# Kernel optimization log

Hardware: AMD Instinct MI355X
Metric: run time of the kernel (lower is better)

## Reference

```python
import jax, jax.numpy as jnp
import numpy as np

N = 4096   # atoms
B = 64     # structures in batch
K = 128    # k-vectors per structure
E = 256    # emb_size_atom
D = 8      # downprojection_size
NUM_HIDDEN = 3


def _silu(x):
    return x * jax.nn.sigmoid(x)


def _residual(x, W):
    # ResidualLayer: two bias-free Dense(E,E) with SiLU, plus skip
    y = _silu(x @ W[0].T)
    y = _silu(y @ W[1].T)
    return x + y


def setup_inputs() -> dict:
    key = jax.random.key(0)
    ks = jax.random.split(key, 10)
    h = jax.random.normal(ks[0], (N, E), jnp.float32)
    x = jax.random.uniform(ks[1], (N, 3), jnp.float32) * 10.0  # Angstrom-scale positions
    k = jax.random.normal(ks[2], (B, K, 3), jnp.float32)
    batch_seg = jnp.sort(jax.random.randint(ks[3], (N,), 0, B))
    sc = 1.0 / np.sqrt(E)
    W_pre = jax.random.normal(ks[4], (2, E, E), jnp.float32) * sc        # pre_residual
    W_down = jax.random.normal(ks[5], (D, K), jnp.float32) / np.sqrt(K)  # shared downprojection (D,K)
    W_up = jax.random.normal(ks[6], (E, D), jnp.float32) / np.sqrt(D)    # up (E,D)
    W0 = jax.random.normal(ks[7], (E, E), jnp.float32) * sc              # first dense of ewald_layers
    W_res = jax.random.normal(ks[8], (NUM_HIDDEN, 2, E, E), jnp.float32) * sc
    return {"h": h, "x": x, "k": k, "batch_seg": batch_seg, "num_batch": B,
            "W_pre": W_pre, "W_down": W_down, "W_up": W_up, "W0": W0, "W_res": W_res}


def reference(h, x, k, batch_seg, num_batch, W_pre, W_down, W_up, W0, W_res):
    hres = _residual(h, W_pre)                       # (N,E)
    # dot products of atom positions with their structure's k-vectors
    dot = jnp.einsum('nkd,nd->nk', k[batch_seg], x)  # (N,K); sinc_damping == 1 (use_pbc)
    c, s = jnp.cos(dot), jnp.sin(dot)
    # structure factors: scatter-sum over atoms within each structure
    sf_real = jax.ops.segment_sum(hres[:, None, :] * c[:, :, None], batch_seg,
                                  num_segments=num_batch)  # (B,K,E)
    sf_imag = jax.ops.segment_sum(hres[:, None, :] * s[:, :, None], batch_seg,
                                  num_segments=num_batch)  # (B,K,E)
    # low-rank learned Fourier-space filter (use_pbc branch)
    kfilter = (W_up @ W_down).T                      # (K,E)
    # re-project filtered structure factors back to atoms
    h_update = 0.01 * jnp.sum(
        (sf_real * kfilter)[batch_seg] * c[:, :, None]
        + (sf_imag * kfilter)[batch_seg] * s[:, :, None], axis=1)  # (N,E)
    # ewald_layers update MLP: Dense + num_hidden residual blocks
    hu = _silu(h_update @ W0.T)
    for i in range(NUM_HIDDEN):
        hu = _residual(hu, W_res[i])
    return hu, dot
```

## Files before the change

kernel.cpp:

```cpp
#include <hip/hip_runtime.h>

#define NN 4096
#define BB 64
#define KK 128
#define EE 256
#define HTS 4352
#define CSR 4224
#define PCAP 160
#define YTS 264
#define ZTS 20

typedef unsigned short u16;
typedef __bf16 bhalf;
typedef bhalf bhalf8 __attribute__((ext_vector_type(8)));
typedef float floatx4 __attribute__((ext_vector_type(4)));

__device__ __forceinline__ float b2f(u16 u) {
  union { unsigned int i; float f; } v; v.i = ((unsigned int)u) << 16; return v.f;
}
__device__ __forceinline__ u16 f2b(float f) {
  union { float f; unsigned int i; } v; v.f = f;
  unsigned int r = (v.i + 0x7FFFu + ((v.i >> 16) & 1u)) >> 16;
  return (u16)r;
}
__device__ __forceinline__ float silu_f(float v) {
  return v / (1.f + __expf(-v));
}
__device__ __forceinline__ bhalf8 ld8f(const float* __restrict__ p) {
  float4 f0 = *(const float4*)p;
  float4 f1 = *(const float4*)(p + 4);
  union { bhalf8 v; u16 s[8]; } u;
  u.s[0] = f2b(f0.x); u.s[1] = f2b(f0.y); u.s[2] = f2b(f0.z); u.s[3] = f2b(f0.w);
  u.s[4] = f2b(f1.x); u.s[5] = f2b(f1.y); u.s[6] = f2b(f1.z); u.s[7] = f2b(f1.w);
  return u.v;
}


__global__ __launch_bounds__(256) void p1_k(
    const float* __restrict__ Wpre, const float* __restrict__ W0,
    const float* __restrict__ Wres, const float* __restrict__ Wup,
    const float* __restrict__ Wdn, const int* __restrict__ bs,
    const float* __restrict__ x, const float* __restrict__ kvec,
    u16* __restrict__ wpre, u16* __restrict__ w0b, u16* __restrict__ wrb,
    float* __restrict__ kft, u16* __restrict__ csb,
    int* __restrict__ seg, float* __restrict__ dout)
{
  int bid = blockIdx.x, tid = threadIdx.x;
  if (bid < 288) {
    int mat = bid >> 5;
    int w8 = ((bid & 31) * 256 + tid);
    int o = w8 * 8;
    int lane = w8 & 63, k = (w8 >> 6) & 7, nt = w8 >> 9;
    int r = lane & 15, q = lane >> 4;
    int src = (nt * 16 + r) * 256 + q * 8 + k * 32;
    const float* S; u16* D;
    if (mat < 2)      { S = Wpre + mat * 65536;       D = wpre + mat * 65536; }
    else if (mat == 2){ S = W0;                       D = w0b; }
    else              { S = Wres + (mat - 3) * 65536; D = wrb + (mat - 3) * 65536; }
    *(bhalf8*)(D + o) = ld8f(S + src);
  }
  else if (bid < 416) {
    int i = (bid - 288) * 256 + tid;
    int e = i >> 7, kk = i & 127;
    float a = 0.f;
#pragma unroll
    for (int d = 0; d < 8; ++d) a += Wup[e * 8 + d] * Wdn[d * KK + kk];
    kft[i] = a;
  } else if (bid < 424) {
    int base = 4096 * 256 + ((bid - 416) * 256 + tid) * 16;
    uint4 z = {0, 0, 0, 0};
    *(uint4*)(csb + base) = z;
    *(uint4*)(csb + base + 8) = z;
  } else if (bid == 424) {
    int b = tid;
    if (b <= BB) {
      int lo = 0, hi = NN;
      while (lo < hi) { int mid = (lo + hi) >> 1; if (bs[mid] < b) lo = mid + 1; else hi = mid; }
      seg[b] = lo;
    }
  } else {
    int i = (bid - 425) * 256 + tid;
    int n = i >> 7, kk = i & 127;
    int b = bs[n];
    const float* kp = kvec + (b * KK + kk) * 3;
    const float* xp = x + n * 3;
    float d = kp[0] * xp[0] + kp[1] * xp[1] + kp[2] * xp[2];
    float sv, cv;
    __sincosf(d, &sv, &cv);
    dout[i] = d;
    csb[(n << 8) + kk] = f2b(cv);
    csb[(n << 8) + 128 + kk] = f2b(sv);
  }
}

__global__ __launch_bounds__(256) void p2_k(
    const float* __restrict__ h, const u16* __restrict__ Wa, const u16* __restrict__ Wb,
    u16* __restrict__ ht,
    const u16* __restrict__ csb, const int* __restrict__ seg, u16* __restrict__ ctb)
{
  __shared__ u16 sh[8256];
  if (blockIdx.x < 256) {
    const int lane = threadIdx.x & 63, wv = threadIdx.x >> 6;
    const int m0 = blockIdx.x * 16;
    const int n0 = wv * 64;
    const int r = lane & 15, q = lane >> 4;
    const int lane8 = lane * 8;
    const float* Ap = h + (m0 + r) * EE + q * 8;
    floatx4 acc[4];
#pragma unroll
    for (int t = 0; t < 4; ++t) acc[t] = (floatx4){0.f, 0.f, 0.f, 0.f};
#pragma unroll
    for (int k = 0; k < 8; ++k) {
      bhalf8 av = ld8f(Ap + k * 32);
#pragma unroll
      for (int t = 0; t < 4; ++t) {
        bhalf8 bv = *(const bhalf8*)(Wa + ((wv * 4 + t) * 8 + k) * 512 + lane8);
        acc[t] = __builtin_amdgcn_mfma_f32_16x16x32_bf16(av, bv, acc[t], 0, 0, 0);
      }
    }
#pragma unroll
    for (int t = 0; t < 4; ++t) {
      int col = n0 + t * 16 + r;
#pragma unroll
      for (int i = 0; i < 4; ++i)
        sh[(q * 4 + i) * YTS + col] = f2b(silu_f(acc[t][i]));
    }
    __syncthreads();
#pragma unroll
    for (int t = 0; t < 4; ++t) acc[t] = (floatx4){0.f, 0.f, 0.f, 0.f};
#pragma unroll
    for (int k = 0; k < 8; ++k) {
      bhalf8 av = *(const bhalf8*)(&sh[r * YTS + q * 8 + k * 32]);
#pragma unroll
      for (int t = 0; t < 4; ++t) {
        bhalf8 bv = *(const bhalf8*)(Wb + ((wv * 4 + t) * 8 + k) * 512 + lane8);
        acc[t] = __builtin_amdgcn_mfma_f32_16x16x32_bf16(av, bv, acc[t], 0, 0, 0);
      }
    }
    __syncthreads();
#pragma unroll
    for (int t = 0; t < 4; ++t) {
      int col = n0 + t * 16 + r;
#pragma unroll
      for (int i = 0; i < 4; ++i) {
        int g = m0 + q * 4 + i;
        float v = silu_f(acc[t][i]) + h[g * EE + col];
        sh[col * ZTS + q * 4 + i] = f2b(v);
      }
    }
    __syncthreads();
    int e = threadIdx.x;
    const uint2* src = (const uint2*)&sh[e * ZTS];
    uint2* dst = (uint2*)(ht + e * HTS + m0);
#pragma unroll
    for (int i = 0; i < 4; ++i) dst[i] = src[i];
  } else {
    int bid2 = blockIdx.x - 256;
    int b = bid2 / 5, p0 = (bid2 % 5) * 32, t = threadIdx.x;
    int s0 = seg[b], s1 = seg[b + 1];
    int abase = s0 & ~7;
#pragma unroll
    for (int it = 0; it < 32; ++it) {
      int idx = it * 256 + t;
      int pl = idx >> 8, j = idx & 255;
      int n = abase + p0 + pl;
      u16 v = 0;
      if (n >= s0 && n < s1) v = csb[(n << 8) | j];
      sh[pl * 258 + j] = v;
    }
    __syncthreads();
    unsigned w[16];
#pragma unroll
    for (int i = 0; i < 16; ++i) {
      unsigned lo = sh[(2 * i) * 258 + t];
      unsigned hi = sh[(2 * i + 1) * 258 + t];
      w[i] = lo | (hi << 16);
    }
    uint4* dst = (uint4*)(ctb + ((b << 8) + t) * PCAP + p0);
#pragma unroll
    for (int i = 0; i < 4; ++i) {
      uint4 u; u.x = w[4*i]; u.y = w[4*i+1]; u.z = w[4*i+2]; u.w = w[4*i+3];
      dst[i] = u;
    }
  }
}

__global__ __launch_bounds__(256) void sf_k(
    const u16* __restrict__ ht, const u16* __restrict__ ctb,
    const float* __restrict__ kft, const int* __restrict__ seg, u16* __restrict__ F)
{
  const int lane = threadIdx.x & 63;
  const int wv = threadIdx.x >> 6;
  const int b = blockIdx.x;
  const int e0 = blockIdx.y * 128 + wv * 32;
  const int j0 = blockIdx.z * 64;
  const int r = lane & 15, q = lane >> 4;
  const int abase = seg[b] & ~7;
  const int phi = seg[b + 1] - abase;
  const u16* Ap = ht + (e0 + r) * HTS + abase + q * 8;
  const u16* Bp = ctb + ((b << 8) + j0 + r) * PCAP + q * 8;
  floatx4 acc[2][4];
#pragma unroll
  for (int m = 0; m < 2; ++m)
#pragma unroll
    for (int t = 0; t < 4; ++t) acc[m][t] = (floatx4){0.f, 0.f, 0.f, 0.f};
  for (int p0 = 0; p0 < phi; p0 += 32) {
    bhalf8 a0 = *(const bhalf8*)(Ap + p0);
    bhalf8 a1 = *(const bhalf8*)(Ap + 16 * HTS + p0);
#pragma unroll
    for (int t = 0; t < 4; ++t) {
      bhalf8 bv = *(const bhalf8*)(Bp + t * 16 * PCAP + p0);
      acc[0][t] = __builtin_amdgcn_mfma_f32_16x16x32_bf16(a0, bv, acc[0][t], 0, 0, 0);
      acc[1][t] = __builtin_amdgcn_mfma_f32_16x16x32_bf16(a1, bv, acc[1][t], 0, 0, 0);
    }
  }
#pragma unroll
  for (int m = 0; m < 2; ++m)
#pragma unroll
    for (int t = 0; t < 4; ++t) {
      int col = j0 + t * 16 + r;
      int kk = col & 127;
#pragma unroll
      for (int i = 0; i < 4; ++i) {
        int row = e0 + m * 16 + q * 4 + i;
        F[((b << 8) + row) * 256 + col] = f2b(acc[m][t][i] * kft[row * KK + kk]);
      }
    }
}

__device__ __forceinline__ void stage2(
    const u16* __restrict__ As, const u16* __restrict__ W,
    u16* __restrict__ Ad, const u16* __restrict__ Ask,
    float* __restrict__ outg, int R0, int c0, int r, int q, int wv, int lane8)
{
  bhalf8 a[8];
#pragma unroll
  for (int k = 0; k < 8; ++k)
    a[k] = *(const bhalf8*)(As + r * YTS + q * 8 + k * 32);
  bhalf8 bf[8][2];
#pragma unroll
  for (int k = 0; k < 8; ++k) {
#pragma unroll
    for (int t = 0; t < 2; ++t)
      bf[k][t] = *(const bhalf8*)(W + ((wv * 2 + t) * 8 + k) * 512 + lane8);
  }
  floatx4 acc[2];
  acc[0] = (floatx4){0.f, 0.f, 0.f, 0.f};
  acc[1] = (floatx4){0.f, 0.f, 0.f, 0.f};
#pragma unroll
  for (int k = 0; k < 8; ++k) {
    acc[0] = __builtin_amdgcn_mfma_f32_16x16x32_bf16(a[k], bf[k][0], acc[0], 0, 0, 0);
    acc[1] = __builtin_amdgcn_mfma_f32_16x16x32_bf16(a[k], bf[k][1], acc[1], 0, 0, 0);
  }
#pragma unroll
  for (int t = 0; t < 2; ++t) {
    int col = c0 + t * 16 + r;
#pragma unroll
    for (int i = 0; i < 4; ++i) {
      int row = q * 4 + i;
      float v = silu_f(acc[t][i]);
      if (Ask) v += b2f(Ask[row * YTS + col]);
      if (outg) outg[(R0 + row) * EE + col] = v;
      else      Ad[row * YTS + col] = f2b(v);
    }
  }
}

__global__ __launch_bounds__(512) void tail_k(
    const u16* __restrict__ csb, const u16* __restrict__ F,
    const int* __restrict__ bs, const int* __restrict__ seg,
    const u16* __restrict__ w0b, const u16* __restrict__ wrb,
    float* __restrict__ out)
{
  __shared__ u16 A0[16 * YTS], A1[16 * YTS];
  const int R0 = blockIdx.x * 16;
  const int lane = threadIdx.x & 63, wv = threadIdx.x >> 6;
  const int r = lane & 15, q = lane >> 4;
  const int c0 = wv * 32;
  const int lane8 = lane * 8;
  {
    const u16* Ap = csb + (R0 + r) * 256 + q * 8;
    bhalf8 a[8];
#pragma unroll
    for (int k = 0; k < 8; ++k) a[k] = *(const bhalf8*)(Ap + k * 32);
    int s = bs[R0];
    while (true) {
      const u16* Bp = F + ((s << 8) + c0 + r) * 256 + q * 8;
      bhalf8 bf[8][2];
#pragma unroll
      for (int k = 0; k < 8; ++k) {
        bf[k][0] = *(const bhalf8*)(Bp + k * 32);
        bf[k][1] = *(const bhalf8*)(Bp + 16 * 256 + k * 32);
      }
      floatx4 acc[2];
      acc[0] = (floatx4){0.f, 0.f, 0.f, 0.f};
      acc[1] = (floatx4){0.f, 0.f, 0.f, 0.f};
#pragma unroll
      for (int k = 0; k < 8; ++k) {
        acc[0] = __builtin_amdgcn_mfma_f32_16x16x32_bf16(a[k], bf[k][0], acc[0], 0, 0, 0);
        acc[1] = __builtin_amdgcn_mfma_f32_16x16x32_bf16(a[k], bf[k][1], acc[1], 0, 0, 0);
      }
      int lo = seg[s] - R0;     if (lo < 0)  lo = 0;
      int hi = seg[s + 1] - R0; if (hi > 16) hi = 16;
#pragma unroll
      for (int t = 0; t < 2; ++t) {
        int col = c0 + t * 16 + r;
#pragma unroll
        for (int i = 0; i < 4; ++i) {
          int row = q * 4 + i;
          if (row >= lo && row < hi)
            A0[row * YTS + col] = f2b(0.01f * acc[t][i]);
        }
      }
      if (seg[s + 1] >= R0 + 16) break;
      ++s;
    }
  }
  __syncthreads();
  stage2(A0, w0b,               A1, nullptr, nullptr, R0, c0, r, q, wv, lane8);
  __syncthreads();
  stage2(A1, wrb + 0 * EE * EE, A0, nullptr, nullptr, R0, c0, r, q, wv, lane8);
  __syncthreads();
  stage2(A0, wrb + 1 * EE * EE, A1, A1,      nullptr, R0, c0, r, q, wv, lane8);
  __syncthreads();
  stage2(A1, wrb + 2 * EE * EE, A0, nullptr, nullptr, R0, c0, r, q, wv, lane8);
  __syncthreads();
  stage2(A0, wrb + 3 * EE * EE, A1, A1,      nullptr, R0, c0, r, q, wv, lane8);
  __syncthreads();
  stage2(A1, wrb + 4 * EE * EE, A0, nullptr, nullptr, R0, c0, r, q, wv, lane8);
  __syncthreads();
  stage2(A0, wrb + 5 * EE * EE, nullptr, A1, out,     R0, c0, r, q, wv, lane8);
}

extern "C" void kernel_launch(void* const* d_in, const int* in_sizes, int n_in,
                              void* d_out, int out_size, void* d_ws, size_t ws_size,
                              hipStream_t stream) {
  const float* h    = (const float*)d_in[0];
  const float* x    = (const float*)d_in[1];
  const float* kv   = (const float*)d_in[2];
  const int*   bs   = (const int*)d_in[3];
  const float* Wpre = (const float*)d_in[5];
  const float* Wdn  = (const float*)d_in[6];
  const float* Wup  = (const float*)d_in[7];
  const float* W0   = (const float*)d_in[8];
  const float* Wres = (const float*)d_in[9];
  float* out = (float*)d_out;

  float* kft = (float*)d_ws;
  int*   seg = (int*)(kft + EE * KK);
  u16* wpre = (u16*)(seg + 128);
  u16* w0b  = wpre + 2 * EE * EE;
  u16* wrb  = w0b + EE * EE;
  u16* csb  = wrb + 6 * EE * EE;
  u16* ctb  = csb + CSR * 256;
  u16* ht   = ctb + BB * 256 * PCAP;
  u16* F    = ht + 256 * HTS;

  p1_k<<<2473, 256, 0, stream>>>(Wpre, W0, Wres, Wup, Wdn, bs, x, kv,
                                 wpre, w0b, wrb, kft, csb, seg, out + NN * EE);
  p2_k<<<576, 256, 0, stream>>>(h, wpre, wpre + EE * EE, ht, csb, seg, ctb);
  sf_k<<<dim3(BB, 2, 4), 256, 0, stream>>>(ht, ctb, kft, seg, F);
  tail_k<<<256, 512, 0, stream>>>(csb, F, bs, seg, w0b, wrb, out);
}
```

Baseline: 123.5 us.

## Fuse four kernels into one cooperative persistent kernel with grid syncs

Replaces the four separate launches (prep, residual/transpose, structure factor, tail MLP) with one cooperative kernel of 256 blocks × 512 threads. Each block runs two 256-thread half-units per phase, and grid.sync() stands in for the kernel boundaries. The aim is to remove per-launch overhead and the tail/drain gaps between kernels. In exchange, occupancy is fixed at 256 blocks and grid-wide barriers are added. Some phases also lose parallelism: the prep phase drops from 2473 blocks to strided passes, and the sf phase now uses 512 half-blocks.

```diff
diff --git a/kernel.cpp b/kernel.cpp
--- a/kernel.cpp
+++ b/kernel.cpp
@@ -1,4 +1,7 @@
 #include <hip/hip_runtime.h>
+#include <hip/hip_cooperative_groups.h>
+
+namespace cg = cooperative_groups;
 
 #define NN 4096
 #define BB 64
@@ -36,7 +39,8 @@
 }
 
 
-__global__ __launch_bounds__(256) void p1_k(
+__device__ __forceinline__ void p0_unit(
+    int bid, int tid,
     const float* __restrict__ Wpre, const float* __restrict__ W0,
     const float* __restrict__ Wres, const float* __restrict__ Wup,
     const float* __restrict__ Wdn, const int* __restrict__ bs,
@@ -45,7 +49,6 @@
     float* __restrict__ kft, u16* __restrict__ csb,
     int* __restrict__ seg, float* __restrict__ dout)
 {
-  int bid = blockIdx.x, tid = threadIdx.x;
   if (bid < 288) {
     int mat = bid >> 5;
     int w8 = ((bid & 31) * 256 + tid);
@@ -93,107 +96,111 @@
   }
 }
 
-__global__ __launch_bounds__(256) void p2_k(
+__device__ __forceinline__ void pair_unit(
+    int u, int tid, u16* __restrict__ sh,
     const float* __restrict__ h, const u16* __restrict__ Wa, const u16* __restrict__ Wb,
-    u16* __restrict__ ht,
+    u16* __restrict__ ht)
+{
+  const int lane = tid & 63, wv = tid >> 6;
+  const int m0 = u * 16;
+  const int n0 = wv * 64;
+  const int r = lane & 15, q = lane >> 4;
+  const int lane8 = lane * 8;
+  const float* Ap = h + (m0 + r) * EE + q * 8;
+  floatx4 acc[4];
+#pragma unroll
+  for (int t = 0; t < 4; ++t) acc[t] = (floatx4){0.f, 0.f, 0.f, 0.f};
+#pragma unroll
+  for (int k = 0; k < 8; ++k) {
+    bhalf8 av = ld8f(Ap + k * 32);
+#pragma unroll
+    for (int t = 0; t < 4; ++t) {
+      bhalf8 bv = *(const bhalf8*)(Wa + ((wv * 4 + t) * 8 + k) * 512 + lane8);
+      acc[t] = __builtin_amdgcn_mfma_f32_16x16x32_bf16(av, bv, acc[t], 0, 0, 0);
+    }
+  }
+#pragma unroll
+  for (int t = 0; t < 4; ++t) {
+    int col = n0 + t * 16 + r;
+#pragma unroll
+    for (int i = 0; i < 4; ++i)
+      sh[(q * 4 + i) * YTS + col] = f2b(silu_f(acc[t][i]));
+  }
+  __syncthreads();
+#pragma unroll
+  for (int t = 0; t < 4; ++t) acc[t] = (floatx4){0.f, 0.f, 0.f, 0.f};
+#pragma unroll
+  for (int k = 0; k < 8; ++k) {
+    bhalf8 av = *(const bhalf8*)(&sh[r * YTS + q * 8 + k * 32]);
+#pragma unroll
+    for (int t = 0; t < 4; ++t) {
+      bhalf8 bv = *(const bhalf8*)(Wb + ((wv * 4 + t) * 8 + k) * 512 + lane8);
+      acc[t] = __builtin_amdgcn_mfma_f32_16x16x32_bf16(av, bv, acc[t], 0, 0, 0);
+    }
+  }
+  __syncthreads();
+#pragma unroll
+  for (int t = 0; t < 4; ++t) {
+    int col = n0 + t * 16 + r;
+#pragma unroll
+    for (int i = 0; i < 4; ++i) {
+      int g = m0 + q * 4 + i;
+      float v = silu_f(acc[t][i]) + h[g * EE + col];
+      sh[col * ZTS + q * 4 + i] = f2b(v);
+    }
+  }
+  __syncthreads();
+  int e = tid;
+  const uint2* src = (const uint2*)&sh[e * ZTS];
+  uint2* dst = (uint2*)(ht + e * HTS + m0);
+#pragma unroll
+  for (int i = 0; i < 4; ++i) dst[i] = src[i];
+}
+
+__device__ __forceinline__ void trans_unit(
+    int u, int t, u16* __restrict__ sh,
     const u16* __restrict__ csb, const int* __restrict__ seg, u16* __restrict__ ctb)
 {
-  __shared__ u16 sh[8256];
-  if (blockIdx.x < 256) {
-    const int lane = threadIdx.x & 63, wv = threadIdx.x >> 6;
-    const int m0 = blockIdx.x * 16;
-    const int n0 = wv * 64;
-    const int r = lane & 15, q = lane >> 4;
-    const int lane8 = lane * 8;
-    const float* Ap = h + (m0 + r) * EE + q * 8;
-    floatx4 acc[4];
-#pragma unroll
-    for (int t = 0; t < 4; ++t) acc[t] = (floatx4){0.f, 0.f, 0.f, 0.f};
-#pragma unroll
-    for (int k = 0; k < 8; ++k) {
-      bhalf8 av = ld8f(Ap + k * 32);
-#pragma unroll
-      for (int t = 0; t < 4; ++t) {
-        bhalf8 bv = *(const bhalf8*)(Wa + ((wv * 4 + t) * 8 + k) * 512 + lane8);
-        acc[t] = __builtin_amdgcn_mfma_f32_16x16x32_bf16(av, bv, acc[t], 0, 0, 0);
-      }
-    }
-#pragma unroll
-    for (int t = 0; t < 4; ++t) {
-      int col = n0 + t * 16 + r;
-#pragma unroll
-      for (int i = 0; i < 4; ++i)
-        sh[(q * 4 + i) * YTS + col] = f2b(silu_f(acc[t][i]));
-    }
-    __syncthreads();
-#pragma unroll
-    for (int t = 0; t < 4; ++t) acc[t] = (floatx4){0.f, 0.f, 0.f, 0.f};
-#pragma unroll
-    for (int k = 0; k < 8; ++k) {
-      bhalf8 av = *(const bhalf8*)(&sh[r * YTS + q * 8 + k * 32]);
-#pragma unroll
-      for (int t = 0; t < 4; ++t) {
-        bhalf8 bv = *(const bhalf8*)(Wb + ((wv * 4 + t) * 8 + k) * 512 + lane8);
-        acc[t] = __builtin_amdgcn_mfma_f32_16x16x32_bf16(av, bv, acc[t], 0, 0, 0);
-      }
-    }
-    __syncthreads();
-#pragma unroll
-    for (int t = 0; t < 4; ++t) {
-      int col = n0 + t * 16 + r;
-#pragma unroll
-      for (int i = 0; i < 4; ++i) {
-        int g = m0 + q * 4 + i;
-        float v = silu_f(acc[t][i]) + h[g * EE + col];
-        sh[col * ZTS + q * 4 + i] = f2b(v);
-      }
-    }
-    __syncthreads();
-    int e = threadIdx.x;
-    const uint2* src = (const uint2*)&sh[e * ZTS];
-    uint2* dst = (uint2*)(ht + e * HTS + m0);
-#pragma unroll
-    for (int i = 0; i < 4; ++i) dst[i] = src[i];
-  } else {
-    int bid2 = blockIdx.x - 256;
-    int b = bid2 / 5, p0 = (bid2 % 5) * 32, t = threadIdx.x;
-    int s0 = seg[b], s1 = seg[b + 1];
-    int abase = s0 & ~7;
-#pragma unroll
-    for (int it = 0; it < 32; ++it) {
-      int idx = it * 256 + t;
-      int pl = idx >> 8, j = idx & 255;
-      int n = abase + p0 + pl;
-      u16 v = 0;
-      if (n >= s0 && n < s1) v = csb[(n << 8) | j];
-      sh[pl * 258 + j] = v;
-    }
-    __syncthreads();
-    unsigned w[16];
-#pragma unroll
-    for (int i = 0; i < 16; ++i) {
-      unsigned lo = sh[(2 * i) * 258 + t];
-      unsigned hi = sh[(2 * i + 1) * 258 + t];
-      w[i] = lo | (hi << 16);
-    }
-    uint4* dst = (uint4*)(ctb + ((b << 8) + t) * PCAP + p0);
-#pragma unroll
-    for (int i = 0; i < 4; ++i) {
-      uint4 u; u.x = w[4*i]; u.y = w[4*i+1]; u.z = w[4*i+2]; u.w = w[4*i+3];
-      dst[i] = u;
-    }
-  }
-}
-
-__global__ __launch_bounds__(256) void sf_k(
+  int b = u / 5, p0 = (u % 5) * 32;
+  int s0 = seg[b], s1 = seg[b + 1];
+  int abase = s0 & ~7;
+#pragma unroll
+  for (int it = 0; it < 32; ++it) {
+    int idx = it * 256 + t;
+    int pl = idx >> 8, j = idx & 255;
+    int n = abase + p0 + pl;
+    u16 v = 0;
+    if (n >= s0 && n < s1) v = csb[(n << 8) | j];
+    sh[pl * 258 + j] = v;
+  }
+  __syncthreads();
+  unsigned w[16];
+#pragma unroll
+  for (int i = 0; i < 16; ++i) {
+    unsigned lo = sh[(2 * i) * 258 + t];
+    unsigned hi = sh[(2 * i + 1) * 258 + t];
+    w[i] = lo | (hi << 16);
+  }
+  uint4* dst = (uint4*)(ctb + ((b << 8) + t) * PCAP + p0);
+#pragma unroll
+  for (int i = 0; i < 4; ++i) {
+    uint4 uu; uu.x = w[4*i]; uu.y = w[4*i+1]; uu.z = w[4*i+2]; uu.w = w[4*i+3];
+    dst[i] = uu;
+  }
+  __syncthreads();
+  __syncthreads();
+}
+
+__device__ __forceinline__ void sf_unit(
+    int u, int tid,
     const u16* __restrict__ ht, const u16* __restrict__ ctb,
     const float* __restrict__ kft, const int* __restrict__ seg, u16* __restrict__ F)
 {
-  const int lane = threadIdx.x & 63;
-  const int wv = threadIdx.x >> 6;
-  const int b = blockIdx.x;
-  const int e0 = blockIdx.y * 128 + wv * 32;
-  const int j0 = blockIdx.z * 64;
+  const int lane = tid & 63, wv = tid >> 6;
+  const int b = u & 63;
+  const int by = (u >> 6) & 1, bz = u >> 7;
+  const int e0 = by * 128 + wv * 32;
+  const int j0 = bz * 64;
   const int r = lane & 15, q = lane >> 4;
   const int abase = seg[b] & ~7;
   const int phi = seg[b + 1] - abase;
@@ -266,15 +273,15 @@
   }
 }
 
-__global__ __launch_bounds__(512) void tail_k(
+__device__ __forceinline__ void tail_body(
+    int blk, int tid, u16* __restrict__ A0, u16* __restrict__ A1,
     const u16* __restrict__ csb, const u16* __restrict__ F,
     const int* __restrict__ bs, const int* __restrict__ seg,
     const u16* __restrict__ w0b, const u16* __restrict__ wrb,
     float* __restrict__ out)
 {
-  __shared__ u16 A0[16 * YTS], A1[16 * YTS];
-  const int R0 = blockIdx.x * 16;
-  const int lane = threadIdx.x & 63, wv = threadIdx.x >> 6;
+  const int R0 = blk * 16;
+  const int lane = tid & 63, wv = tid >> 6;
   const int r = lane & 15, q = lane >> 4;
   const int c0 = wv * 32;
   const int lane8 = lane * 8;
@@ -330,6 +337,46 @@
   stage2(A1, wrb + 4 * EE * EE, A0, nullptr, nullptr, R0, c0, r, q, wv, lane8);
   __syncthreads();
   stage2(A0, wrb + 5 * EE * EE, nullptr, A1, out,     R0, c0, r, q, wv, lane8);
+}
+
+__global__ __launch_bounds__(512) void mega_k(
+    const float* __restrict__ h, const float* __restrict__ x,
+    const float* __restrict__ kv, const int* __restrict__ bs,
+    const float* __restrict__ Wpre, const float* __restrict__ Wdn,
+    const float* __restrict__ Wup, const float* __restrict__ W0,
+    const float* __restrict__ Wres,
+    u16* __restrict__ wpre, u16* __restrict__ w0b, u16* __restrict__ wrb,
+    float* __restrict__ kft, u16* __restrict__ csb, int* __restrict__ seg,
+    u16* __restrict__ ctb, u16* __restrict__ ht, u16* __restrict__ F,
+    float* __restrict__ out)
+{
+  __shared__ u16 SH[16512];
+  cg::grid_group grid = cg::this_grid();
+  const int blk = blockIdx.x, tid = threadIdx.x;
+  const int half = tid >> 8, t2 = tid & 255;
+
+#pragma unroll
+  for (int pass = 0; pass < 5; ++pass) {
+    int bid = pass * 512 + blk * 2 + half;
+    if (bid < 2473)
+      p0_unit(bid, t2, Wpre, W0, Wres, Wup, Wdn, bs, x, kv,
+              wpre, w0b, wrb, kft, csb, seg, out + NN * EE);
+  }
+  grid.sync();
+
+  for (int pass = 0; pass < 2; ++pass) {
+    int u = pass * 512 + blk * 2 + half;
+    u16* sh = SH + half * 8256;
+    if (u < 256)      pair_unit(u, t2, sh, h, wpre, wpre + EE * EE, ht);
+    else if (u < 576) trans_unit(u - 256, t2, sh, csb, seg, ctb);
+    else { __syncthreads(); __syncthreads(); __syncthreads(); }
+  }
+  grid.sync();
+
+  sf_unit(blk * 2 + half, t2, ht, ctb, kft, seg, F);
+  grid.sync();
+
+  tail_body(blk, tid, SH, SH + 4224, csb, F, bs, seg, w0b, wrb, out);
 }
 
 extern "C" void kernel_launch(void* const* d_in, const int* in_sizes, int n_in,
@@ -356,9 +403,8 @@
   u16* ht   = ctb + BB * 256 * PCAP;
   u16* F    = ht + 256 * HTS;
 
-  p1_k<<<2473, 256, 0, stream>>>(Wpre, W0, Wres, Wup, Wdn, bs, x, kv,
-                                 wpre, w0b, wrb, kft, csb, seg, out + NN * EE);
-  p2_k<<<576, 256, 0, stream>>>(h, wpre, wpre + EE * EE, ht, csb, seg, ctb);
-  sf_k<<<dim3(BB, 2, 4), 256, 0, stream>>>(ht, ctb, kft, seg, F);
-  tail_k<<<256, 512, 0, stream>>>(csb, F, bs, seg, w0b, wrb, out);
-}
+  void* args[] = {&h, &x, &kv, &bs, &Wpre, &Wdn, &Wup, &W0, &Wres,
+                  &wpre, &w0b, &wrb, &kft, &csb, &seg, &ctb, &ht, &F, &out};
+  hipLaunchCooperativeKernel((const void*)mega_k, dim3(256), dim3(512),
+                             args, 0, stream);
+}
```

Result: slower. 248.0 us (+100.8%).
